# Optimization experiments

Measured on AMD Instinct MI355X. Metric: run time of the kernel, lower is better.

## Reference

```python
import jax, jax.numpy as jnp
import numpy as np

HEADS = 4
HEAD_DIM = 24
PH, PW = 2, 2  # proposal grid -> M = PH*PW = 4 prototype centers
EPS = 1e-12


def setup_inputs() -> dict:
    key = jax.random.key(0)
    ks = jax.random.split(key, 6)
    B, Cin, H, W = 16, 128, 112, 112
    Cout = 128
    D = HEADS * HEAD_DIM  # 96
    x = jax.random.normal(ks[0], (B, Cin, H, W), jnp.float32)
    # 1x1 conv weights stored as [out, in] (kernel dims squeezed)
    f_w = jax.random.normal(ks[1], (D, Cin), jnp.float32) / np.float32(np.sqrt(Cin))
    f_b = jnp.zeros((D,), jnp.float32)
    v_w = jax.random.normal(ks[2], (D, Cin), jnp.float32) / np.float32(np.sqrt(Cin))
    v_b = jnp.zeros((D,), jnp.float32)
    proj_w = jax.random.normal(ks[3], (Cout, D), jnp.float32) / np.float32(np.sqrt(D))
    proj_b = jnp.zeros((Cout,), jnp.float32)
    sim_alpha = jnp.ones((1,), jnp.float32)
    sim_beta = jnp.zeros((1,), jnp.float32)
    # OrthogonalPriorGenerator: Gram-Schmidt orthonormalized random rows
    rng = np.random.default_rng(0)
    W0 = rng.standard_normal((HEAD_DIM, PH * PW)).astype(np.float32) * np.sqrt(2.0 / HEAD_DIM).astype(np.float32)
    q, _ = np.linalg.qr(W0)  # orthonormal columns
    centers = jnp.asarray(q.T, jnp.float32)  # [M, head_dim], orthonormal rows
    return {"x": x, "f_w": f_w, "f_b": f_b, "v_w": v_w, "v_b": v_b,
            "proj_w": proj_w, "proj_b": proj_b,
            "sim_alpha": sim_alpha, "sim_beta": sim_beta, "centers": centers}


def reference(x, f_w, f_b, v_w, v_b, proj_w, proj_b, sim_alpha, sim_beta, centers):
    B, Cin, H, W = x.shape
    M = PH * PW
    c = HEAD_DIM
    bh = B * HEADS
    n = H * W
    # 1x1 convs
    f = jnp.einsum('oi,bihw->bohw', f_w, x) + f_b[None, :, None, None]
    v = jnp.einsum('oi,bihw->bohw', v_w, x) + v_b[None, :, None, None]
    # split heads into batch: b (e c) h w -> (b e) c h w
    f = f.reshape(bh, c, n)                      # [(be), c, n]
    v4 = v.reshape(bh, c, H, W)                  # [(be), c, h, w]
    # adaptive avg pool to (PH, PW) -> value centers [(be), M, c]
    vc = v4.reshape(bh, c, PH, H // PH, PW, W // PW).mean(axis=(3, 5))
    value_centers = vc.reshape(bh, c, M).transpose(0, 2, 1)
    # cosine similarity of orthonormal centers vs tokens
    cn = centers / jnp.maximum(jnp.linalg.norm(centers, axis=-1, keepdims=True), EPS)
    xn = f.transpose(0, 2, 1)                    # [(be), n, c]
    xn = xn / jnp.maximum(jnp.linalg.norm(xn, axis=-1, keepdims=True), EPS)
    sim = jax.nn.sigmoid(sim_beta + sim_alpha * jnp.einsum('mc,bnc->bmn', cn, xn))
    # hard top-1 assignment mask over centers
    idx = jnp.argmax(sim, axis=1)                # [(be), n]
    mask = jax.nn.one_hot(idx, M, axis=1, dtype=sim.dtype)  # [(be), M, n]
    sim = sim * mask
    # dispatch: weighted aggregation into centers
    value2 = v4.reshape(bh, c, n).transpose(0, 2, 1)          # [(be), n, c]
    agg = (jnp.einsum('bmn,bnc->bmc', sim, value2) + value_centers)
    agg = agg / (sim.sum(axis=-1, keepdims=True) + 1.0)
    # combine: redistribute center features back to tokens
    out = jnp.einsum('bmn,bmc->bnc', sim, agg)                # [(be), n, c]
    out = out.transpose(0, 2, 1).reshape(B, HEADS * c, H, W)  # merge heads
    out = jnp.einsum('oi,bihw->bohw', proj_w, out) + proj_b[None, :, None, None]
    assignment_map = idx[0].reshape(H, W)
    return out, assignment_map
```

## Files before the change

kernel.cpp:

```cpp
#include <hip/hip_runtime.h>
#include <hip/hip_bf16.h>

namespace {

constexpr int kCin   = 128;
constexpr int kHW    = 12544;
constexpr int kW     = 112;
constexpr int kGrps  = 49;
constexpr int kTiles = 196;
constexpr size_t kOut1Off = (size_t)16 * 128 * kHW;

__device__ __forceinline__ float bf2f(unsigned short u) {
  union { unsigned int i; float f; } v;
  v.i = ((unsigned int)u) << 16;
  return v.f;
}

__device__ __forceinline__ unsigned short f2bf(float f) {
  union { float f; unsigned int i; } v;
  v.f = f;
  unsigned int x = v.i;
  x += 0x7fffu + ((x >> 16) & 1u);
  return (unsigned short)(x >> 16);
}

template <bool BF>
__device__ __forceinline__ float ld1(const void* p, size_t i) {
  if constexpr (BF) return bf2f(((const unsigned short*)p)[i]);
  else              return ((const float*)p)[i];
}
template <bool BF>
__device__ __forceinline__ void ld4(const void* p, size_t i, float o[4]) {
  if constexpr (BF) {
    const ushort4 u = *reinterpret_cast<const ushort4*>((const unsigned short*)p + i);
    o[0] = bf2f(u.x); o[1] = bf2f(u.y); o[2] = bf2f(u.z); o[3] = bf2f(u.w);
  } else {
    const float4 u = *reinterpret_cast<const float4*>((const float*)p + i);
    o[0] = u.x; o[1] = u.y; o[2] = u.z; o[3] = u.w;
  }
}
template <bool BF>
__device__ __forceinline__ void st1(void* p, size_t i, float v) {
  if constexpr (BF) ((unsigned short*)p)[i] = f2bf(v);
  else              ((float*)p)[i] = v;
}

__global__ void detect_dtype(const unsigned short* __restrict__ fw, int* __restrict__ flag) {
  __shared__ int cnt_s;
  if (threadIdx.x == 0) cnt_s = 0;
  __syncthreads();
  int c = 0;
  for (int i = threadIdx.x; i < 4096; i += 256) {
    const float v = bf2f(fw[i]);
    if (fabsf(v) > 4.0f) ++c;
  }
  atomicAdd(&cnt_s, c);
  __syncthreads();
  if (threadIdx.x == 0) flag[0] = (cnt_s > 100) ? 0 : 1;
}

struct SMain {
  float fh[96 * 65];
  float cn[4][24];
  float s[4][64];
  unsigned char idx[4][64];
  unsigned char q[64];
};

template <bool BF>
__device__ __forceinline__ void main_body(
    SMain& sm,
    const void* __restrict__ x,  const void* __restrict__ f_w, const void* __restrict__ f_b,
    const void* __restrict__ v_w, const void* __restrict__ v_b,
    const void* __restrict__ sim_alpha, const void* __restrict__ sim_beta,
    const void* __restrict__ centers,
    void* __restrict__ out0,
    float* __restrict__ aggsum, float* __restrict__ vpool, float* __restrict__ cnt)
{
  const int tid  = threadIdx.x;
  const int b    = blockIdx.x / kTiles;
  const int tile = blockIdx.x % kTiles;
  const int hw0  = tile * 64;

  if (tid < 4) {
    float cv[24];
    float n2 = 0.f;
#pragma unroll
    for (int c = 0; c < 24; ++c) { cv[c] = ld1<BF>(centers, tid * 24 + c); n2 += cv[c] * cv[c]; }
    const float inv = 1.f / fmaxf(sqrtf(n2), 1e-12f);
#pragma unroll
    for (int c = 0; c < 24; ++c) sm.cn[tid][c] = cv[c] * inv;
  }
  const float alpha = ld1<BF>(sim_alpha, 0);
  const float beta  = ld1<BF>(sim_beta, 0);

  const int ty = tid >> 4;
  const int tx = tid & 15;
  const bool is_f = (ty < 8);
  const void*  wsel  = is_f ? f_w : v_w;
  const void*  bsel  = is_f ? f_b : v_b;
  const size_t wrow0 = (size_t)(is_f ? ty * 12 : ty * 12 - 96);
  float bias[12];
#pragma unroll
  for (int r = 0; r < 12; ++r) bias[r] = ld1<BF>(bsel, wrow0 + r);

  const int e   = tid >> 6;
  const int tok = tid & 63;

  __syncthreads();

  float acc[12][4];
#pragma unroll
  for (int r = 0; r < 12; ++r)
#pragma unroll
    for (int j = 0; j < 4; ++j) acc[r][j] = 0.f;

  const size_t xbase = ((size_t)b * kCin) * kHW + hw0 + tx * 4;
  for (int i = 0; i < 128; i += 4) {
    float xv[4][4];
#pragma unroll
    for (int ci = 0; ci < 4; ++ci) ld4<BF>(x, xbase + (size_t)(i + ci) * kHW, xv[ci]);
    float wv[6][4];
#pragma unroll
    for (int r = 0; r < 6; ++r) ld4<BF>(wsel, (wrow0 + r) * 128 + i, wv[r]);
#pragma unroll
    for (int r = 0; r < 6; ++r)
#pragma unroll
      for (int ci = 0; ci < 4; ++ci)
#pragma unroll
        for (int j = 0; j < 4; ++j)
          acc[r][j] = fmaf(wv[r][ci], xv[ci][j], acc[r][j]);
#pragma unroll
    for (int r = 0; r < 6; ++r) ld4<BF>(wsel, (wrow0 + 6 + r) * 128 + i, wv[r]);
#pragma unroll
    for (int r = 0; r < 6; ++r)
#pragma unroll
      for (int ci = 0; ci < 4; ++ci)
#pragma unroll
        for (int j = 0; j < 4; ++j)
          acc[6 + r][j] = fmaf(wv[r][ci], xv[ci][j], acc[6 + r][j]);
  }

  if (is_f) {
#pragma unroll
    for (int r = 0; r < 12; ++r)
#pragma unroll
      for (int j = 0; j < 4; ++j)
        sm.fh[(ty * 12 + r) * 65 + tx * 4 + j] = acc[r][j] + bias[r];
  }
  __syncthreads();

  {
    float dm[4] = {0.f, 0.f, 0.f, 0.f};
    float n2 = 0.f;
#pragma unroll
    for (int c = 0; c < 24; ++c) {
      const float fc = sm.fh[(e * 24 + c) * 65 + tok];
      n2 += fc * fc;
      dm[0] += fc * sm.cn[0][c];
      dm[1] += fc * sm.cn[1][c];
      dm[2] += fc * sm.cn[2][c];
      dm[3] += fc * sm.cn[3][c];
    }
    const float inv = 1.f / fmaxf(sqrtf(n2), 1e-12f);
    float s[4];
#pragma unroll
    for (int m = 0; m < 4; ++m) {
      const float z = beta + alpha * dm[m] * inv;
      s[m] = 1.f / (1.f + __expf(-z));
    }
    float best = -1.f;
    int bi = 0;
#pragma unroll
    for (int m = 0; m < 4; ++m)
      if (s[m] > best) { best = s[m]; bi = m; }

    const int hw = hw0 + tok;
    st1<BF>(out0, ((size_t)(b * 128 + e)) * kHW + hw, best);
    st1<BF>(out0, ((size_t)(b * 128 + 4 + e)) * kHW + hw, (float)bi);
    sm.s[e][tok]   = best;
    sm.idx[e][tok] = (unsigned char)bi;
    if (e == 0) {
      const int h = hw / kW;
      const int w = hw - h * kW;
      sm.q[tok] = (unsigned char)((h >= 56 ? 2 : 0) + (w >= 56 ? 1 : 0));
    }
  }
  __syncthreads();

  if (!is_f) {
#pragma unroll
    for (int r = 0; r < 12; ++r)
#pragma unroll
      for (int j = 0; j < 4; ++j)
        sm.fh[((ty - 8) * 12 + r) * 65 + tx * 4 + j] = acc[r][j] + bias[r];
  }
  __syncthreads();

  float agg_m[4]  = {0.f, 0.f, 0.f, 0.f};
  float pool_q[4] = {0.f, 0.f, 0.f, 0.f};
  float cacc = 0.f;
  if (tid < 192) {
    const int half = tid / 96;
    const int c    = tid - half * 96;
    const int eh   = c / 24;
    const int row0 = c * 65;
    const int t20  = half * 32;
    for (int k = 0; k < 32; ++k) {
      const int t2 = t20 + k;
      const float v = sm.fh[row0 + t2];
      const float s = sm.s[eh][t2];
      const int  mi = sm.idx[eh][t2];
      const int  q  = sm.q[t2];
      const float sv = s * v;
      agg_m[0]  += (mi == 0) ? sv : 0.f;
      agg_m[1]  += (mi == 1) ? sv : 0.f;
      agg_m[2]  += (mi == 2) ? sv : 0.f;
      agg_m[3]  += (mi == 3) ? sv : 0.f;
      pool_q[0] += (q == 0) ? v : 0.f;
      pool_q[1] += (q == 1) ? v : 0.f;
      pool_q[2] += (q == 2) ? v : 0.f;
      pool_q[3] += (q == 3) ? v : 0.f;
    }
    const int cc  = c % 24;
    const int bh  = b * 4 + eh;
#pragma unroll
    for (int m = 0; m < 4; ++m) {
      atomicAdd(&aggsum[(bh * 4 + m) * 24 + cc], agg_m[m]);
      atomicAdd(&vpool[(bh * 4 + m) * 24 + cc], pool_q[m]);
    }
  } else if (tid < 224) {
    const int p  = tid - 192;
    const int em = p >> 1;
    const int ce = em >> 2, cm = em & 3;
    const int t20 = (p & 1) * 32;
    for (int k = 0; k < 32; ++k) {
      const int t2 = t20 + k;
      cacc += (sm.idx[ce][t2] == cm) ? sm.s[ce][t2] : 0.f;
    }
    atomicAdd(&cnt[b * 16 + em], cacc);
  }
}

__global__ __launch_bounds__(256, 4) void cluster_main(
    const int* __restrict__ flag,
    const void* x, const void* f_w, const void* f_b, const void* v_w, const void* v_b,
    const void* sim_alpha, const void* sim_beta, const void* centers,
    void* out0, float* aggsum, float* vpool, float* cnt)
{
  __shared__ SMain sm;
  if (*flag)
    main_body<true>(sm, x, f_w, f_b, v_w, v_b, sim_alpha, sim_beta, centers, out0, aggsum, vpool, cnt);
  else
    main_body<false>(sm, x, f_w, f_b, v_w, v_b, sim_alpha, sim_beta, centers, out0, aggsum, vpool, cnt);
}

template <bool BF>
__device__ __forceinline__ void ptab_body(
    float* __restrict__ af, const void* __restrict__ proj_w,
    const float* __restrict__ aggsum, const float* __restrict__ vpool,
    const float* __restrict__ cnt, float* __restrict__ ptab)
{
  const int b   = blockIdx.x;
  const int tid = threadIdx.x;
  for (int k = tid; k < 384; k += 256) {
    const int em = k / 24;
    af[k] = (aggsum[b * 384 + k] + vpool[b * 384 + k] * (1.f / 3136.f)) / (cnt[b * 16 + em] + 1.f);
  }
  __syncthreads();
#pragma unroll
  for (int i = 0; i < 8; ++i) {
    const int g  = i * 256 + tid;
    const int o  = g >> 4;
    const int em = g & 15;
    const int e  = em >> 2;
    float acc = 0.f;
#pragma unroll
    for (int c = 0; c < 24; ++c)
      acc = fmaf(ld1<BF>(proj_w, (size_t)o * 96 + e * 24 + c), af[em * 24 + c], acc);
    ptab[b * 2048 + g] = acc;
  }
}

__global__ void cluster_ptab(const int* __restrict__ flag, const void* proj_w,
                             const float* __restrict__ aggsum, const float* __restrict__ vpool,
                             const float* __restrict__ cnt, float* __restrict__ ptab) {
  __shared__ float af[384];
  if (*flag) ptab_body<true>(af, proj_w, aggsum, vpool, cnt, ptab);
  else       ptab_body<false>(af, proj_w, aggsum, vpool, cnt, ptab);
}

struct SOut {
  float p[2048];
  float pb[128];
};

template <bool BF>
__device__ __forceinline__ void out_body(
    SOut& so, const float* __restrict__ ptab,
    const void* __restrict__ proj_b, void* __restrict__ out0)
{
  const int tid = threadIdx.x;
  const int b   = blockIdx.x / kGrps;
  const int grp = blockIdx.x % kGrps;
  const int hw  = grp * 256 + tid;

  for (int k = tid; k < 2048; k += 256) so.p[k] = ptab[b * 2048 + k];
  if (tid < 128) so.pb[tid] = ld1<BF>(proj_b, tid);
  __syncthreads();

  const size_t base = ((size_t)(b * 128)) * kHW + hw;
  float sv[4];
  int   mi[4];
  float iv0 = 0.f;
#pragma unroll
  for (int e = 0; e < 4; ++e) {
    sv[e] = ld1<BF>(out0, base + (size_t)e * kHW);
    const float iv = ld1<BF>(out0, base + (size_t)(4 + e) * kHW);
    if (e == 0) iv0 = iv;
    mi[e] = (int)(iv + 0.5f);
  }
  if (b == 0) {
    st1<BF>(out0, kOut1Off + hw, iv0);
  }

#pragma unroll 4
  for (int o = 0; o < 128; ++o) {
    float a = so.pb[o];
    a = fmaf(sv[0], so.p[o * 16 +  0 + mi[0]], a);
    a = fmaf(sv[1], so.p[o * 16 +  4 + mi[1]], a);
    a = fmaf(sv[2], so.p[o * 16 +  8 + mi[2]], a);
    a = fmaf(sv[3], so.p[o * 16 + 12 + mi[3]], a);
    st1<BF>(out0, base + (size_t)o * kHW, a);
  }
}

__global__ __launch_bounds__(256) void cluster_out(
    const int* __restrict__ flag,
    const void* proj_b, const float* __restrict__ ptab, void* out0)
{
  __shared__ SOut so;
  if (*flag) out_body<true>(so, ptab, proj_b, out0);
  else       out_body<false>(so, ptab, proj_b, out0);
}

}

extern "C" void kernel_launch(void* const* d_in, const int* in_sizes, int n_in,
                              void* d_out, int out_size, void* d_ws, size_t ws_size,
                              hipStream_t stream) {
  const void* x         = d_in[0];
  const void* f_w       = d_in[1];
  const void* f_b       = d_in[2];
  const void* v_w       = d_in[3];
  const void* v_b       = d_in[4];
  const void* proj_w    = d_in[5];
  const void* proj_b    = d_in[6];
  const void* sim_alpha = d_in[7];
  const void* sim_beta  = d_in[8];
  const void* centers   = d_in[9];

  int*   flag   = (int*)d_ws;
  float* fws    = (float*)((char*)d_ws + 16);
  float* aggsum = fws;
  float* vpool  = fws + 6144;
  float* cnt    = fws + 12288;
  float* ptab   = fws + 12544;

  hipMemsetAsync(d_ws, 0, 16 + 12544 * sizeof(float), stream);

  detect_dtype<<<dim3(1), dim3(256), 0, stream>>>((const unsigned short*)f_w, flag);
  cluster_main<<<dim3(16 * kTiles), dim3(256), 0, stream>>>(
      flag, x, f_w, f_b, v_w, v_b, sim_alpha, sim_beta, centers,
      d_out, aggsum, vpool, cnt);
  cluster_ptab<<<dim3(16), dim3(256), 0, stream>>>(flag, proj_w, aggsum, vpool, cnt, ptab);
  cluster_out<<<dim3(16 * kGrps), dim3(256), 0, stream>>>(flag, proj_b, ptab, d_out);
}
```

Baseline: 493.4 us.

## Stage conv weights and input tiles in shared memory for the fused 1x1 convs

The fused f/v 1x1 conv loop now loads 32-channel chunks of both weight matrices and the 64-token input tile cooperatively into LDS, then runs the register-blocked FMA loop from shared memory. Before, each thread read weights and x straight from global memory. That meant many redundant weight loads across threads and uncoalesced strided x reads. The LDS staging buffer shares a union with the later fh buffer. The cost is two extra barriers per chunk, a larger LDS footprint that may lower occupancy, and the removal of the early barrier before the centers are used.

```diff
diff --git a/kernel.cpp b/kernel.cpp
--- a/kernel.cpp
+++ b/kernel.cpp
@@ -59,8 +59,14 @@
   if (threadIdx.x == 0) flag[0] = (cnt_s > 100) ? 0 : 1;
 }
 
-struct SMain {
-  float fh[96 * 65];
+struct alignas(16) SMain {
+  union {
+    struct {
+      float w[192 * 36];
+      float x[32 * 64];
+    } a;
+    float fh[96 * 65];
+  } u;
   float cn[4][24];
   float s[4][64];
   unsigned char idx[4][64];
@@ -97,17 +103,15 @@
   const int ty = tid >> 4;
   const int tx = tid & 15;
   const bool is_f = (ty < 8);
-  const void*  wsel  = is_f ? f_w : v_w;
   const void*  bsel  = is_f ? f_b : v_b;
   const size_t wrow0 = (size_t)(is_f ? ty * 12 : ty * 12 - 96);
   float bias[12];
 #pragma unroll
   for (int r = 0; r < 12; ++r) bias[r] = ld1<BF>(bsel, wrow0 + r);
 
-  const int e   = tid >> 6;
-  const int tok = tid & 63;
-
-  __syncthreads();
+  const int e     = tid >> 6;
+  const int tok   = tid & 63;
+  const int lrow0 = ty * 12;
 
   float acc[12][4];
 #pragma unroll
@@ -115,30 +119,65 @@
 #pragma unroll
     for (int j = 0; j < 4; ++j) acc[r][j] = 0.f;
 
-  const size_t xbase = ((size_t)b * kCin) * kHW + hw0 + tx * 4;
-  for (int i = 0; i < 128; i += 4) {
-    float xv[4][4];
-#pragma unroll
-    for (int ci = 0; ci < 4; ++ci) ld4<BF>(x, xbase + (size_t)(i + ci) * kHW, xv[ci]);
-    float wv[6][4];
-#pragma unroll
-    for (int r = 0; r < 6; ++r) ld4<BF>(wsel, (wrow0 + r) * 128 + i, wv[r]);
-#pragma unroll
-    for (int r = 0; r < 6; ++r)
-#pragma unroll
-      for (int ci = 0; ci < 4; ++ci)
-#pragma unroll
-        for (int j = 0; j < 4; ++j)
-          acc[r][j] = fmaf(wv[r][ci], xv[ci][j], acc[r][j]);
-#pragma unroll
-    for (int r = 0; r < 6; ++r) ld4<BF>(wsel, (wrow0 + 6 + r) * 128 + i, wv[r]);
-#pragma unroll
-    for (int r = 0; r < 6; ++r)
-#pragma unroll
-      for (int ci = 0; ci < 4; ++ci)
-#pragma unroll
-        for (int j = 0; j < 4; ++j)
-          acc[6 + r][j] = fmaf(wv[r][ci], xv[ci][j], acc[6 + r][j]);
+  for (int c0 = 0; c0 < 128; c0 += 32) {
+#pragma unroll
+    for (int s = 0; s < 6; ++s) {
+      const int u2  = tid + 256 * s;
+      const int row = u2 >> 3;
+      const int cg  = u2 & 7;
+      float t4[4];
+      if (row < 96) ld4<BF>(f_w, (size_t)row * 128 + c0 + cg * 4, t4);
+      else          ld4<BF>(v_w, (size_t)(row - 96) * 128 + c0 + cg * 4, t4);
+      *reinterpret_cast<float4*>(&sm.u.a.w[row * 36 + cg * 4]) =
+          make_float4(t4[0], t4[1], t4[2], t4[3]);
+    }
+#pragma unroll
+    for (int s = 0; s < 2; ++s) {
+      const int u2 = tid + 256 * s;
+      const int ch = u2 >> 4;
+      const int tg = u2 & 15;
+      float t4[4];
+      ld4<BF>(x, ((size_t)b * kCin + c0 + ch) * kHW + hw0 + tg * 4, t4);
+      *reinterpret_cast<float4*>(&sm.u.a.x[ch * 64 + tg * 4]) =
+          make_float4(t4[0], t4[1], t4[2], t4[3]);
+    }
+    __syncthreads();
+
+#pragma unroll
+    for (int kk = 0; kk < 32; kk += 4) {
+      float xr[4][4];
+#pragma unroll
+      for (int ci = 0; ci < 4; ++ci) {
+        const float4 v4 = *reinterpret_cast<const float4*>(&sm.u.a.x[(kk + ci) * 64 + tx * 4]);
+        xr[ci][0] = v4.x; xr[ci][1] = v4.y; xr[ci][2] = v4.z; xr[ci][3] = v4.w;
+      }
+      float wr[6][4];
+#pragma unroll
+      for (int r = 0; r < 6; ++r) {
+        const float4 v4 = *reinterpret_cast<const float4*>(&sm.u.a.w[(lrow0 + r) * 36 + kk]);
+        wr[r][0] = v4.x; wr[r][1] = v4.y; wr[r][2] = v4.z; wr[r][3] = v4.w;
+      }
+#pragma unroll
+      for (int r = 0; r < 6; ++r)
+#pragma unroll
+        for (int ci = 0; ci < 4; ++ci)
+#pragma unroll
+          for (int j = 0; j < 4; ++j)
+            acc[r][j] = fmaf(wr[r][ci], xr[ci][j], acc[r][j]);
+#pragma unroll
+      for (int r = 0; r < 6; ++r) {
+        const float4 v4 = *reinterpret_cast<const float4*>(&sm.u.a.w[(lrow0 + 6 + r) * 36 + kk]);
+        wr[r][0] = v4.x; wr[r][1] = v4.y; wr[r][2] = v4.z; wr[r][3] = v4.w;
+      }
+#pragma unroll
+      for (int r = 0; r < 6; ++r)
+#pragma unroll
+        for (int ci = 0; ci < 4; ++ci)
+#pragma unroll
+          for (int j = 0; j < 4; ++j)
+            acc[6 + r][j] = fmaf(wr[r][ci], xr[ci][j], acc[6 + r][j]);
+    }
+    __syncthreads();
   }
 
   if (is_f) {
@@ -146,7 +185,7 @@
     for (int r = 0; r < 12; ++r)
 #pragma unroll
       for (int j = 0; j < 4; ++j)
-        sm.fh[(ty * 12 + r) * 65 + tx * 4 + j] = acc[r][j] + bias[r];
+        sm.u.fh[(ty * 12 + r) * 65 + tx * 4 + j] = acc[r][j] + bias[r];
   }
   __syncthreads();
 
@@ -155,7 +194,7 @@
     float n2 = 0.f;
 #pragma unroll
     for (int c = 0; c < 24; ++c) {
-      const float fc = sm.fh[(e * 24 + c) * 65 + tok];
+      const float fc = sm.u.fh[(e * 24 + c) * 65 + tok];
       n2 += fc * fc;
       dm[0] += fc * sm.cn[0][c];
       dm[1] += fc * sm.cn[1][c];
@@ -193,7 +232,7 @@
     for (int r = 0; r < 12; ++r)
 #pragma unroll
       for (int j = 0; j < 4; ++j)
-        sm.fh[((ty - 8) * 12 + r) * 65 + tx * 4 + j] = acc[r][j] + bias[r];
+        sm.u.fh[((ty - 8) * 12 + r) * 65 + tx * 4 + j] = acc[r][j] + bias[r];
   }
   __syncthreads();
 
@@ -208,7 +247,7 @@
     const int t20  = half * 32;
     for (int k = 0; k < 32; ++k) {
       const int t2 = t20 + k;
-      const float v = sm.fh[row0 + t2];
+      const float v = sm.u.fh[row0 + t2];
       const float s = sm.s[eh][t2];
       const int  mi = sm.idx[eh][t2];
       const int  q  = sm.q[t2];
```

Result: faster. 481.9 us (-2.3%).

## Use bf16 MFMA for 1x1 conv, fuse ptab into output kernel, vectorize stores

Applied to the files above, without the earlier changes.

For bf16 inputs, the f/v 1x1 projection now stages an x tile transposed in shared memory and computes it with 16x16x32 bf16 MFMA instructions instead of scalar FMAs. The separate ptab kernel is folded into the output kernel, so each output block recomputes the small projection table itself. The output kernel is restructured so each thread handles 8 tokens across 16 channels with vectorized loads and stores. The changes cut ALU work and one launch, at the cost of redundant ptab computation per block and lower occupancy (launch bounds changed from 4 to 2).

```diff
diff --git a/kernel.cpp b/kernel.cpp
--- a/kernel.cpp
+++ b/kernel.cpp
@@ -9,6 +9,9 @@
 constexpr int kGrps  = 49;
 constexpr int kTiles = 196;
 constexpr size_t kOut1Off = (size_t)16 * 128 * kHW;
+
+typedef __attribute__((ext_vector_type(8))) short short8;
+typedef __attribute__((ext_vector_type(4))) float f32x4;
 
 __device__ __forceinline__ float bf2f(unsigned short u) {
   union { unsigned int i; float f; } v;
@@ -44,6 +47,18 @@
   if constexpr (BF) ((unsigned short*)p)[i] = f2bf(v);
   else              ((float*)p)[i] = v;
 }
+template <bool BF>
+__device__ __forceinline__ void st4(void* p, size_t i, const float v[4]) {
+  if constexpr (BF) {
+    ushort4 u;
+    u.x = f2bf(v[0]); u.y = f2bf(v[1]); u.z = f2bf(v[2]); u.w = f2bf(v[3]);
+    *reinterpret_cast<ushort4*>((unsigned short*)p + i) = u;
+  } else {
+    float4 u;
+    u.x = v[0]; u.y = v[1]; u.z = v[2]; u.w = v[3];
+    *reinterpret_cast<float4*>((float*)p + i) = u;
+  }
+}
 
 __global__ void detect_dtype(const unsigned short* __restrict__ fw, int* __restrict__ flag) {
   __shared__ int cnt_s;
@@ -59,8 +74,11 @@
   if (threadIdx.x == 0) flag[0] = (cnt_s > 100) ? 0 : 1;
 }
 
-struct SMain {
-  float fh[96 * 65];
+struct alignas(16) SMain {
+  union {
+    unsigned short xt[64][136];
+    float fh[96 * 65];
+  } u;
   float cn[4][24];
   float s[4][64];
   unsigned char idx[4][64];
@@ -94,59 +112,127 @@
   const float alpha = ld1<BF>(sim_alpha, 0);
   const float beta  = ld1<BF>(sim_beta, 0);
 
+  const int e   = tid >> 6;
+  const int tok = tid & 63;
+
+  const int lane = tid & 63;
+  const int wv   = tid >> 6;
+  const int qq   = lane >> 4;
+  const int tt   = lane & 15;
+  f32x4 accB[3][4];
+  float biasB[3][4];
+  int   wrb = 0;
+  bool  isfB = true;
+
   const int ty = tid >> 4;
   const int tx = tid & 15;
   const bool is_f = (ty < 8);
-  const void*  wsel  = is_f ? f_w : v_w;
-  const void*  bsel  = is_f ? f_b : v_b;
-  const size_t wrow0 = (size_t)(is_f ? ty * 12 : ty * 12 - 96);
+  float acc[12][4];
   float bias[12];
-#pragma unroll
-  for (int r = 0; r < 12; ++r) bias[r] = ld1<BF>(bsel, wrow0 + r);
-
-  const int e   = tid >> 6;
-  const int tok = tid & 63;
-
-  __syncthreads();
-
-  float acc[12][4];
-#pragma unroll
-  for (int r = 0; r < 12; ++r)
-#pragma unroll
-    for (int j = 0; j < 4; ++j) acc[r][j] = 0.f;
-
-  const size_t xbase = ((size_t)b * kCin) * kHW + hw0 + tx * 4;
-  for (int i = 0; i < 128; i += 4) {
-    float xv[4][4];
-#pragma unroll
-    for (int ci = 0; ci < 4; ++ci) ld4<BF>(x, xbase + (size_t)(i + ci) * kHW, xv[ci]);
-    float wv[6][4];
-#pragma unroll
-    for (int r = 0; r < 6; ++r) ld4<BF>(wsel, (wrow0 + r) * 128 + i, wv[r]);
-#pragma unroll
-    for (int r = 0; r < 6; ++r)
-#pragma unroll
-      for (int ci = 0; ci < 4; ++ci)
+
+  if constexpr (BF) {
+#pragma unroll
+    for (int s5 = 0; s5 < 8; ++s5) {
+      const int id2 = tid + s5 * 256;
+      const int ch  = id2 >> 4;
+      const int tg  = id2 & 15;
+      const ushort4 u4 = *reinterpret_cast<const ushort4*>(
+          (const unsigned short*)x + ((size_t)b * kCin + ch) * kHW + hw0 + tg * 4);
+      sm.u.xt[tg * 4 + 0][ch] = u4.x;
+      sm.u.xt[tg * 4 + 1][ch] = u4.y;
+      sm.u.xt[tg * 4 + 2][ch] = u4.z;
+      sm.u.xt[tg * 4 + 3][ch] = u4.w;
+    }
+    const int wbase = wv * 48;
+    isfB = (wv < 2);
+    const unsigned short* wselB = (const unsigned short*)(isfB ? f_w : v_w);
+    const void* bselB = isfB ? f_b : v_b;
+    wrb = isfB ? wbase : wbase - 96;
+#pragma unroll
+    for (int rt = 0; rt < 3; ++rt)
+#pragma unroll
+      for (int rg = 0; rg < 4; ++rg)
+        biasB[rt][rg] = ld1<true>(bselB, (size_t)(wrb + rt * 16 + qq * 4 + rg));
+    __syncthreads();
+
+    const f32x4 z4 = {0.f, 0.f, 0.f, 0.f};
+#pragma unroll
+    for (int rt = 0; rt < 3; ++rt)
+#pragma unroll
+      for (int ct = 0; ct < 4; ++ct) accB[rt][ct] = z4;
+
+#pragma unroll
+    for (int rt = 0; rt < 3; ++rt) {
+      short8 afr[4];
+#pragma unroll
+      for (int k = 0; k < 4; ++k)
+        afr[k] = *reinterpret_cast<const short8*>(
+            wselB + (size_t)(wrb + rt * 16 + tt) * 128 + k * 32 + qq * 8);
+#pragma unroll
+      for (int ct = 0; ct < 4; ++ct) {
+#pragma unroll
+        for (int k = 0; k < 4; ++k) {
+          const short8 bfr = *reinterpret_cast<const short8*>(
+              &sm.u.xt[ct * 16 + tt][k * 32 + qq * 8]);
+          accB[rt][ct] = __builtin_amdgcn_mfma_f32_16x16x32_bf16(afr[k], bfr, accB[rt][ct], 0, 0, 0);
+        }
+      }
+    }
+    __syncthreads();
+
+    if (isfB) {
+#pragma unroll
+      for (int rt = 0; rt < 3; ++rt)
+#pragma unroll
+        for (int ct = 0; ct < 4; ++ct)
+#pragma unroll
+          for (int rg = 0; rg < 4; ++rg)
+            sm.u.fh[(wrb + rt * 16 + qq * 4 + rg) * 65 + ct * 16 + tt] =
+                accB[rt][ct][rg] + biasB[rt][rg];
+    }
+  } else {
+    const void*  wsel  = is_f ? f_w : v_w;
+    const void*  bsel  = is_f ? f_b : v_b;
+    const size_t wrow0 = (size_t)(is_f ? ty * 12 : ty * 12 - 96);
+#pragma unroll
+    for (int r = 0; r < 12; ++r) bias[r] = ld1<false>(bsel, wrow0 + r);
+#pragma unroll
+    for (int r = 0; r < 12; ++r)
+#pragma unroll
+      for (int j = 0; j < 4; ++j) acc[r][j] = 0.f;
+
+    const size_t xbase = ((size_t)b * kCin) * kHW + hw0 + tx * 4;
+    for (int i = 0; i < 128; i += 4) {
+      float xv[4][4];
+#pragma unroll
+      for (int ci = 0; ci < 4; ++ci) ld4<false>(x, xbase + (size_t)(i + ci) * kHW, xv[ci]);
+      float wvr[6][4];
+#pragma unroll
+      for (int r = 0; r < 6; ++r) ld4<false>(wsel, (wrow0 + r) * 128 + i, wvr[r]);
+#pragma unroll
+      for (int r = 0; r < 6; ++r)
+#pragma unroll
+        for (int ci = 0; ci < 4; ++ci)
+#pragma unroll
+          for (int j = 0; j < 4; ++j)
+            acc[r][j] = fmaf(wvr[r][ci], xv[ci][j], acc[r][j]);
+#pragma unroll
+      for (int r = 0; r < 6; ++r) ld4<false>(wsel, (wrow0 + 6 + r) * 128 + i, wvr[r]);
+#pragma unroll
+      for (int r = 0; r < 6; ++r)
+#pragma unroll
+        for (int ci = 0; ci < 4; ++ci)
+#pragma unroll
+          for (int j = 0; j < 4; ++j)
+            acc[6 + r][j] = fmaf(wvr[r][ci], xv[ci][j], acc[6 + r][j]);
+    }
+    if (is_f) {
+#pragma unroll
+      for (int r = 0; r < 12; ++r)
 #pragma unroll
         for (int j = 0; j < 4; ++j)
-          acc[r][j] = fmaf(wv[r][ci], xv[ci][j], acc[r][j]);
-#pragma unroll
-    for (int r = 0; r < 6; ++r) ld4<BF>(wsel, (wrow0 + 6 + r) * 128 + i, wv[r]);
-#pragma unroll
-    for (int r = 0; r < 6; ++r)
-#pragma unroll
-      for (int ci = 0; ci < 4; ++ci)
-#pragma unroll
-        for (int j = 0; j < 4; ++j)
-          acc[6 + r][j] = fmaf(wv[r][ci], xv[ci][j], acc[6 + r][j]);
-  }
-
-  if (is_f) {
-#pragma unroll
-    for (int r = 0; r < 12; ++r)
-#pragma unroll
-      for (int j = 0; j < 4; ++j)
-        sm.fh[(ty * 12 + r) * 65 + tx * 4 + j] = acc[r][j] + bias[r];
+          sm.u.fh[(ty * 12 + r) * 65 + tx * 4 + j] = acc[r][j] + bias[r];
+    }
   }
   __syncthreads();
 
@@ -155,7 +241,7 @@
     float n2 = 0.f;
 #pragma unroll
     for (int c = 0; c < 24; ++c) {
-      const float fc = sm.fh[(e * 24 + c) * 65 + tok];
+      const float fc = sm.u.fh[(e * 24 + c) * 65 + tok];
       n2 += fc * fc;
       dm[0] += fc * sm.cn[0][c];
       dm[1] += fc * sm.cn[1][c];
@@ -188,12 +274,25 @@
   }
   __syncthreads();
 
-  if (!is_f) {
-#pragma unroll
-    for (int r = 0; r < 12; ++r)
-#pragma unroll
-      for (int j = 0; j < 4; ++j)
-        sm.fh[((ty - 8) * 12 + r) * 65 + tx * 4 + j] = acc[r][j] + bias[r];
+  if constexpr (BF) {
+    if (!isfB) {
+#pragma unroll
+      for (int rt = 0; rt < 3; ++rt)
+#pragma unroll
+        for (int ct = 0; ct < 4; ++ct)
+#pragma unroll
+          for (int rg = 0; rg < 4; ++rg)
+            sm.u.fh[(wrb + rt * 16 + qq * 4 + rg) * 65 + ct * 16 + tt] =
+                accB[rt][ct][rg] + biasB[rt][rg];
+    }
+  } else {
+    if (!is_f) {
+#pragma unroll
+      for (int r = 0; r < 12; ++r)
+#pragma unroll
+        for (int j = 0; j < 4; ++j)
+          sm.u.fh[((ty - 8) * 12 + r) * 65 + tx * 4 + j] = acc[r][j] + bias[r];
+    }
   }
   __syncthreads();
 
@@ -208,7 +307,7 @@
     const int t20  = half * 32;
     for (int k = 0; k < 32; ++k) {
       const int t2 = t20 + k;
-      const float v = sm.fh[row0 + t2];
+      const float v = sm.u.fh[row0 + t2];
       const float s = sm.s[eh][t2];
       const int  mi = sm.idx[eh][t2];
       const int  q  = sm.q[t2];
@@ -242,7 +341,7 @@
   }
 }
 
-__global__ __launch_bounds__(256, 4) void cluster_main(
+__global__ __launch_bounds__(256, 2) void cluster_main(
     const int* __restrict__ flag,
     const void* x, const void* f_w, const void* f_b, const void* v_w, const void* v_b,
     const void* sim_alpha, const void* sim_beta, const void* centers,
@@ -255,18 +354,27 @@
     main_body<false>(sm, x, f_w, f_b, v_w, v_b, sim_alpha, sim_beta, centers, out0, aggsum, vpool, cnt);
 }
 
-template <bool BF>
-__device__ __forceinline__ void ptab_body(
-    float* __restrict__ af, const void* __restrict__ proj_w,
+struct SOut {
+  float af[384];
+  float p[2048];
+  float pb[128];
+};
+
+template <bool BF>
+__device__ __forceinline__ void out_body(
+    SOut& so, const void* __restrict__ proj_w, const void* __restrict__ proj_b,
     const float* __restrict__ aggsum, const float* __restrict__ vpool,
-    const float* __restrict__ cnt, float* __restrict__ ptab)
+    const float* __restrict__ cnt, void* __restrict__ out0)
 {
-  const int b   = blockIdx.x;
   const int tid = threadIdx.x;
+  const int b   = blockIdx.x / kGrps;
+  const int grp = blockIdx.x % kGrps;
+
   for (int k = tid; k < 384; k += 256) {
     const int em = k / 24;
-    af[k] = (aggsum[b * 384 + k] + vpool[b * 384 + k] * (1.f / 3136.f)) / (cnt[b * 16 + em] + 1.f);
-  }
+    so.af[k] = (aggsum[b * 384 + k] + vpool[b * 384 + k] * (1.f / 3136.f)) / (cnt[b * 16 + em] + 1.f);
+  }
+  if (tid < 128) so.pb[tid] = ld1<BF>(proj_b, tid);
   __syncthreads();
 #pragma unroll
   for (int i = 0; i < 8; ++i) {
@@ -274,74 +382,71 @@
     const int o  = g >> 4;
     const int em = g & 15;
     const int e  = em >> 2;
-    float acc = 0.f;
+    float a = 0.f;
 #pragma unroll
     for (int c = 0; c < 24; ++c)
-      acc = fmaf(ld1<BF>(proj_w, (size_t)o * 96 + e * 24 + c), af[em * 24 + c], acc);
-    ptab[b * 2048 + g] = acc;
-  }
-}
-
-__global__ void cluster_ptab(const int* __restrict__ flag, const void* proj_w,
-                             const float* __restrict__ aggsum, const float* __restrict__ vpool,
-                             const float* __restrict__ cnt, float* __restrict__ ptab) {
-  __shared__ float af[384];
-  if (*flag) ptab_body<true>(af, proj_w, aggsum, vpool, cnt, ptab);
-  else       ptab_body<false>(af, proj_w, aggsum, vpool, cnt, ptab);
-}
-
-struct SOut {
-  float p[2048];
-  float pb[128];
-};
-
-template <bool BF>
-__device__ __forceinline__ void out_body(
-    SOut& so, const float* __restrict__ ptab,
-    const void* __restrict__ proj_b, void* __restrict__ out0)
-{
-  const int tid = threadIdx.x;
-  const int b   = blockIdx.x / kGrps;
-  const int grp = blockIdx.x % kGrps;
-  const int hw  = grp * 256 + tid;
-
-  for (int k = tid; k < 2048; k += 256) so.p[k] = ptab[b * 2048 + k];
-  if (tid < 128) so.pb[tid] = ld1<BF>(proj_b, tid);
-  __syncthreads();
-
+      a = fmaf(ld1<BF>(proj_w, (size_t)o * 96 + e * 24 + c), so.af[em * 24 + c], a);
+    so.p[g] = a;
+  }
+  __syncthreads();
+
+  const int tgi = tid & 31;
+  const int cg  = tid >> 5;
+  const int hw  = grp * 256 + tgi * 8;
   const size_t base = ((size_t)(b * 128)) * kHW + hw;
-  float sv[4];
-  int   mi[4];
-  float iv0 = 0.f;
-#pragma unroll
-  for (int e = 0; e < 4; ++e) {
-    sv[e] = ld1<BF>(out0, base + (size_t)e * kHW);
-    const float iv = ld1<BF>(out0, base + (size_t)(4 + e) * kHW);
-    if (e == 0) iv0 = iv;
-    mi[e] = (int)(iv + 0.5f);
-  }
-  if (b == 0) {
-    st1<BF>(out0, kOut1Off + hw, iv0);
-  }
-
-#pragma unroll 4
-  for (int o = 0; o < 128; ++o) {
-    float a = so.pb[o];
-    a = fmaf(sv[0], so.p[o * 16 +  0 + mi[0]], a);
-    a = fmaf(sv[1], so.p[o * 16 +  4 + mi[1]], a);
-    a = fmaf(sv[2], so.p[o * 16 +  8 + mi[2]], a);
-    a = fmaf(sv[3], so.p[o * 16 + 12 + mi[3]], a);
-    st1<BF>(out0, base + (size_t)o * kHW, a);
+
+  float sv[4][8];
+  int   mi[4][8];
+  float ivh[8];
+#pragma unroll
+  for (int e2 = 0; e2 < 4; ++e2) {
+    ld4<BF>(out0, base + (size_t)e2 * kHW,     &sv[e2][0]);
+    ld4<BF>(out0, base + (size_t)e2 * kHW + 4, &sv[e2][4]);
+    float iv[8];
+    ld4<BF>(out0, base + (size_t)(4 + e2) * kHW,     &iv[0]);
+    ld4<BF>(out0, base + (size_t)(4 + e2) * kHW + 4, &iv[4]);
+#pragma unroll
+    for (int j = 0; j < 8; ++j) {
+      mi[e2][j] = (int)(iv[j] + 0.5f);
+      if (e2 == 0) ivh[j] = iv[j];
+    }
+  }
+  __syncthreads();
+
+  if (b == 0 && cg == 0) {
+    st4<BF>(out0, kOut1Off + hw,     &ivh[0]);
+    st4<BF>(out0, kOut1Off + hw + 4, &ivh[4]);
+  }
+
+#pragma unroll
+  for (int oi = 0; oi < 16; ++oi) {
+    const int o = cg * 16 + oi;
+    const float* pr  = &so.p[o * 16];
+    const float  pbv = so.pb[o];
+    float ov[8];
+#pragma unroll
+    for (int j = 0; j < 8; ++j) {
+      float a = pbv;
+      a = fmaf(sv[0][j], pr[ 0 + mi[0][j]], a);
+      a = fmaf(sv[1][j], pr[ 4 + mi[1][j]], a);
+      a = fmaf(sv[2][j], pr[ 8 + mi[2][j]], a);
+      a = fmaf(sv[3][j], pr[12 + mi[3][j]], a);
+      ov[j] = a;
+    }
+    st4<BF>(out0, base + (size_t)o * kHW,     &ov[0]);
+    st4<BF>(out0, base + (size_t)o * kHW + 4, &ov[4]);
   }
 }
 
 __global__ __launch_bounds__(256) void cluster_out(
     const int* __restrict__ flag,
-    const void* proj_b, const float* __restrict__ ptab, void* out0)
+    const void* proj_w, const void* proj_b,
+    const float* __restrict__ aggsum, const float* __restrict__ vpool,
+    const float* __restrict__ cnt, void* out0)
 {
   __shared__ SOut so;
-  if (*flag) out_body<true>(so, ptab, proj_b, out0);
-  else       out_body<false>(so, ptab, proj_b, out0);
+  if (*flag) out_body<true>(so, proj_w, proj_b, aggsum, vpool, cnt, out0);
+  else       out_body<false>(so, proj_w, proj_b, aggsum, vpool, cnt, out0);
 }
 
 }
@@ -365,7 +470,6 @@
   float* aggsum = fws;
   float* vpool  = fws + 6144;
   float* cnt    = fws + 12288;
-  float* ptab   = fws + 12544;
 
   hipMemsetAsync(d_ws, 0, 16 + 12544 * sizeof(float), stream);
 
@@ -373,6 +477,6 @@
   cluster_main<<<dim3(16 * kTiles), dim3(256), 0, stream>>>(
       flag, x, f_w, f_b, v_w, v_b, sim_alpha, sim_beta, centers,
       d_out, aggsum, vpool, cnt);
-  cluster_ptab<<<dim3(16), dim3(256), 0, stream>>>(flag, proj_w, aggsum, vpool, cnt, ptab);
-  cluster_out<<<dim3(16 * kGrps), dim3(256), 0, stream>>>(flag, proj_b, ptab, d_out);
-}
+  cluster_out<<<dim3(16 * kGrps), dim3(256), 0, stream>>>(
+      flag, proj_w, proj_b, aggsum, vpool, cnt, d_out);
+}
```

Measured after the change: 486.4 us. No clear change (-1.4%).
